# Kernel optimization log

Measured on AMD Instinct MI355X. Metric: run time of the kernel, lower is better.

The kernel has to match this reference:

```python
import jax, jax.numpy as jnp
import numpy as np
from jax import lax

BS, DIM, S, CF, K = 8, 128, 1024, 512, 16384
TAU = 0.2
EPS = 1e-12


def _norm(x, axis):
    # torch F.normalize: x / max(||x||, eps)
    return x / jnp.clip(jnp.linalg.norm(x, axis=axis, keepdims=True), EPS, None)


def setup_inputs() -> dict:
    key = jax.random.key(0)
    ks = jax.random.split(key, 8)
    inp = {
        "g_q": jax.random.normal(ks[0], (BS, DIM), jnp.float32),
        "g_k": jax.random.normal(ks[1], (BS, DIM), jnp.float32),
        "d_q": jax.random.normal(ks[2], (BS, DIM, S), jnp.float32),
        "d_k": jax.random.normal(ks[3], (BS, DIM, S), jnp.float32),
        "feat_q": jax.random.normal(ks[4], (BS, CF, S), jnp.float32),
        "feat_k": jax.random.normal(ks[5], (BS, CF, S), jnp.float32),
        # queues are L2-normalized along dim 0 at module construction
        "queue_g": _norm(jax.random.normal(ks[6], (DIM, K), jnp.float32), 0),
        "queue_d": _norm(jax.random.normal(ks[7], (DIM, K), jnp.float32), 0),
    }
    return inp


def reference(g_q, g_k, d_q, d_k, feat_q, feat_k, queue_g, queue_d):
    g_qn = _norm(g_q, 1)                      # [B, D]
    d_qn = _norm(d_q, 1)                      # [B, D, S]

    # --- torch.no_grad() block: key branch + dense 1-NN match ---
    g_kn = _norm(g_k, 1)                      # [B, D]
    d_kn = _norm(d_k, 1)                      # [B, D, S]
    f_k = _norm(feat_k, 1)                    # [B, C, S]
    f_q = _norm(feat_q, 1)                    # [B, C, S]
    cosine = jnp.einsum('bqi,bqj->bij', f_k, f_q)   # [B, S, S]
    match_idx = jnp.argmax(cosine, axis=1)          # [B, S]
    # gather query dense features at matched indices (detached, as in source)
    d_qg = jnp.take_along_axis(d_qn, match_idx[:, None, :], axis=2)  # [B, D, S]
    g_kn, d_kn, d_qg = lax.stop_gradient((g_kn, d_kn, d_qg))

    # global contrastive logits
    pos_g = jnp.einsum('bd,bd->b', g_qn, g_kn)[:, None]              # [B, 1]
    neg_g = g_qn @ lax.stop_gradient(queue_g)                        # [B, K]
    output_g = jnp.concatenate([pos_g, neg_g], axis=1) / TAU         # [B, 1+K]
    target_g = jnp.zeros((BS,), dtype=jnp.int32)

    # dense contrastive logits
    pos_d = jnp.einsum('bdz,bdz->bz', d_kn, d_qg)[:, None, :]        # [B, 1, S]
    neg_d = jnp.einsum('bdz,dq->bqz', d_qg, lax.stop_gradient(queue_d))  # [B, K, S]
    output_d = jnp.concatenate([pos_d, neg_d], axis=1) / TAU         # [B, 1+K, S]
    target_d = jnp.zeros((BS, S), dtype=jnp.int32)

    return output_g, target_g, output_d, target_d
```

## Files before the change

kernel.cpp:

```cpp
#include <hip/hip_runtime.h>
#include <math.h>
#include <stdint.h>

constexpr int B   = 8;
constexpr int DIM = 128;
constexpr int S   = 1024;
constexpr int CF  = 512;
constexpr int K   = 16384;
constexpr float INV_TAU = 5.0f;
constexpr float EPSF    = 1e-12f;

constexpr int64_t OG_OFF = 0;
constexpr int64_t TG_OFF = (int64_t)B * (K + 1);
constexpr int64_t OD_OFF = TG_OFF + B;
constexpr int64_t TD_OFF = OD_OFF + (int64_t)B * (K + 1) * S;

typedef __attribute__((ext_vector_type(8))) short s16x8;
typedef __attribute__((ext_vector_type(4))) float f32x4;

__device__ inline void split2(float x, uint16_t& h, uint16_t& l) {
    uint32_t bx = __float_as_uint(x);
    h = (uint16_t)(bx >> 16);
    float r = x - __uint_as_float(bx & 0xFFFF0000u);
    l = (uint16_t)(__float_as_uint(r) >> 16);
}

__global__ void zero_targets_kernel(float* out) {
    int t = blockIdx.x * 256 + threadIdx.x;
    if (t < B) out[TG_OFF + t] = 0.0f;
    if (t < B * S) out[TD_OFF + t] = 0.0f;
}

__global__ void g_norm_kernel(const float* __restrict__ g_q,
                              const float* __restrict__ g_k,
                              float* __restrict__ g_qn,
                              float* __restrict__ g_kn,
                              float* __restrict__ out) {
    int b = blockIdx.x;
    int d = threadIdx.x;
    float q = g_q[b * DIM + d];
    float k = g_k[b * DIM + d];
    float sq = q * q, sk = k * k;
#pragma unroll
    for (int off = 32; off > 0; off >>= 1) {
        sq += __shfl_down(sq, off, 64);
        sk += __shfl_down(sk, off, 64);
    }
    __shared__ float red[4];
    int w = d >> 6;
    if ((d & 63) == 0) { red[w] = sq; red[2 + w] = sk; }
    __syncthreads();
    float invq = 1.0f / fmaxf(sqrtf(red[0] + red[1]), EPSF);
    float invk = 1.0f / fmaxf(sqrtf(red[2] + red[3]), EPSF);
    float qn = q * invq, kn = k * invk;
    g_qn[b * DIM + d] = qn;
    g_kn[b * DIM + d] = kn;
    float p = qn * kn;
#pragma unroll
    for (int off = 32; off > 0; off >>= 1) p += __shfl_down(p, off, 64);
    __shared__ float red2[2];
    if ((d & 63) == 0) red2[w] = p;
    __syncthreads();
    if (d == 0) out[OG_OFF + (int64_t)b * (K + 1)] = (red2[0] + red2[1]) * INV_TAU;
}

__global__ void neg_g_kernel(const float* __restrict__ g_qn,
                             const float* __restrict__ queue_g,
                             float* __restrict__ out) {
    __shared__ float gq[B * DIM];
    int t = threadIdx.x;
    for (int i = t; i < B * DIM; i += 256) gq[i] = g_qn[i];
    __syncthreads();
    int k = blockIdx.x * 256 + t;
    float acc[B] = {0, 0, 0, 0, 0, 0, 0, 0};
    for (int d = 0; d < DIM; ++d) {
        float v = queue_g[(int64_t)d * K + k];
#pragma unroll
        for (int b = 0; b < B; ++b) acc[b] = fmaf(gq[b * DIM + d], v, acc[b]);
    }
#pragma unroll
    for (int b = 0; b < B; ++b)
        out[OG_OFF + (int64_t)b * (K + 1) + 1 + k] = acc[b] * INV_TAU;
}

template <int ROWS>
__global__ void invnorm_kernel(const float* __restrict__ x, float* __restrict__ rn) {
    int b = blockIdx.y;
    int s = blockIdx.x * 64 + (threadIdx.x & 63);
    int g = threadIdx.x >> 6;
    const float* base = x + (int64_t)b * ROWS * S + s;
    float acc = 0.0f;
    for (int r = g; r < ROWS; r += 4) {
        float v = base[(int64_t)r * S];
        acc = fmaf(v, v, acc);
    }
    __shared__ float red[256];
    red[threadIdx.x] = acc;
    __syncthreads();
    if (g == 0) {
        int sl = threadIdx.x;
        float tot = red[sl] + red[64 + sl] + red[128 + sl] + red[192 + sl];
        rn[b * S + s] = 1.0f / fmaxf(sqrtf(tot), EPSF);
    }
}

constexpr int CC = 32;
__global__ void cos_argmax_kernel(const float* __restrict__ f_k,
                                  const float* __restrict__ f_q,
                                  const float* __restrict__ rn_fk,
                                  const float* __restrict__ rn_fq,
                                  float* __restrict__ pmax,
                                  int* __restrict__ pidx) {
    int jt = blockIdx.x, ic = blockIdx.y, b = blockIdx.z;
    int j0 = jt * 64;
    int tx = threadIdx.x & 15, ty = threadIdx.x >> 4;
    __shared__ __align__(16) float sk[CC][68];
    __shared__ __align__(16) float sq[CC][68];
    const float* fkb = f_k + (int64_t)b * CF * S;
    const float* fqb = f_q + (int64_t)b * CF * S;

    float bestv[4];
    int besti[4];
#pragma unroll
    for (int jj = 0; jj < 4; ++jj) { bestv[jj] = -INFINITY; besti[jj] = 0; }
    float rq[4];
#pragma unroll
    for (int jj = 0; jj < 4; ++jj) rq[jj] = rn_fq[b * S + j0 + ty * 4 + jj];

    for (int it = 0; it < 4; ++it) {
        int i_base = ic * 256 + it * 64;
        float acc[4][4] = {};
        for (int c0 = 0; c0 < CF; c0 += CC) {
            for (int e = threadIdx.x; e < CC * 64; e += 256) {
                int r = e >> 6, col = e & 63;
                sk[r][col] = fkb[(int64_t)(c0 + r) * S + i_base + col];
                sq[r][col] = fqb[(int64_t)(c0 + r) * S + j0 + col];
            }
            __syncthreads();
#pragma unroll
            for (int r = 0; r < CC; ++r) {
                float4 av4 = *(const float4*)&sk[r][tx * 4];
                float4 bv4 = *(const float4*)&sq[r][ty * 4];
                float a_[4] = {av4.x, av4.y, av4.z, av4.w};
                float b_[4] = {bv4.x, bv4.y, bv4.z, bv4.w};
#pragma unroll
                for (int ii = 0; ii < 4; ++ii)
#pragma unroll
                    for (int jj = 0; jj < 4; ++jj)
                        acc[ii][jj] = fmaf(a_[ii], b_[jj], acc[ii][jj]);
            }
            __syncthreads();
        }
        float rk[4];
#pragma unroll
        for (int ii = 0; ii < 4; ++ii) rk[ii] = rn_fk[b * S + i_base + tx * 4 + ii];
#pragma unroll
        for (int jj = 0; jj < 4; ++jj)
#pragma unroll
            for (int ii = 0; ii < 4; ++ii) {
                float v = acc[ii][jj] * rk[ii] * rq[jj];
                if (v > bestv[jj]) { bestv[jj] = v; besti[jj] = i_base + tx * 4 + ii; }
            }
    }
#pragma unroll
    for (int jj = 0; jj < 4; ++jj) {
        float v = bestv[jj];
        int idx = besti[jj];
#pragma unroll
        for (int off = 8; off > 0; off >>= 1) {
            float ov = __shfl_down(v, off, 16);
            int oi = __shfl_down(idx, off, 16);
            if (ov > v || (ov == v && oi < idx)) { v = ov; idx = oi; }
        }
        if (tx == 0) {
            int j = j0 + ty * 4 + jj;
            pmax[(int64_t)(ic * B + b) * S + j] = v;
            pidx[(int64_t)(ic * B + b) * S + j] = idx;
        }
    }
}

__global__ void argmax_merge_kernel(const float* __restrict__ pmax,
                                    const int* __restrict__ pidx,
                                    int* __restrict__ match) {
    int t = blockIdx.x * 256 + threadIdx.x;
    if (t >= B * S) return;
    int b = t / S, s = t % S;
    float bv = -INFINITY;
    int bi = 0;
    for (int ic = 0; ic < 4; ++ic) {
        float v = pmax[(int64_t)(ic * B + b) * S + s];
        int i = pidx[(int64_t)(ic * B + b) * S + s];
        if (v > bv || (v == bv && i < bi)) { bv = v; bi = i; }
    }
    match[t] = bi;
}

__global__ void queue_split_kernel(const float* __restrict__ qd,
                                   uint16_t* __restrict__ qhi,
                                   uint16_t* __restrict__ qlo) {
    int q0 = blockIdx.x * 64;
    __shared__ float tile[DIM][65];
    for (int e = threadIdx.x; e < DIM * 64; e += 256) {
        int d = e >> 6, c = e & 63;
        tile[d][c] = qd[(int64_t)d * K + q0 + c];
    }
    __syncthreads();
    int qq = threadIdx.x >> 2;
    int dg = threadIdx.x & 3;
    uint16_t* gh = qhi + (int64_t)(q0 + qq) * DIM + dg * 32;
    uint16_t* gl = qlo + (int64_t)(q0 + qq) * DIM + dg * 32;
#pragma unroll
    for (int v = 0; v < 4; ++v) {
        uint32_t ph[4], pl[4];
#pragma unroll
        for (int p = 0; p < 4; ++p) {
            int d = dg * 32 + v * 8 + p * 2;
            uint16_t h0, l0, h1, l1;
            split2(tile[d][qq], h0, l0);
            split2(tile[d + 1][qq], h1, l1);
            ph[p] = (uint32_t)h0 | ((uint32_t)h1 << 16);
            pl[p] = (uint32_t)l0 | ((uint32_t)l1 << 16);
        }
        *(uint4*)(gh + v * 8) = make_uint4(ph[0], ph[1], ph[2], ph[3]);
        *(uint4*)(gl + v * 8) = make_uint4(pl[0], pl[1], pl[2], pl[3]);
    }
}

__global__ void gather_prep_kernel(const float* __restrict__ d_q,
                                   const float* __restrict__ d_k,
                                   const float* __restrict__ rn_dq,
                                   const int* __restrict__ match,
                                   uint16_t* __restrict__ ghi,
                                   uint16_t* __restrict__ glo,
                                   float* __restrict__ out) {
    int b = blockIdx.y, z0 = blockIdx.x * 64;
    int zl = threadIdx.x & 63, dg = threadIdx.x >> 6;
    __shared__ float tile[DIM][65];
    __shared__ float redd[4][64], redn[4][64];
    __shared__ int   sm[64];
    __shared__ float ssc[64];
    if (threadIdx.x < 64) {
        int m = match[b * S + z0 + threadIdx.x];
        sm[threadIdx.x] = m;
        ssc[threadIdx.x] = rn_dq[b * S + m];
    }
    __syncthreads();
    int m = sm[zl];
    float sc = ssc[zl];
    const float* dqb = d_q + (int64_t)b * DIM * S;
    const float* dkb = d_k + (int64_t)b * DIM * S + z0;
    float dot = 0.0f, nk = 0.0f;
    for (int i = 0; i < 32; ++i) {
        int d = dg * 32 + i;
        float val = dqb[(int64_t)d * S + m] * sc;
        float kv  = dkb[(int64_t)d * S + zl];
        tile[d][zl] = val;
        dot = fmaf(kv, val, dot);
        nk  = fmaf(kv, kv, nk);
    }
    redd[dg][zl] = dot;
    redn[dg][zl] = nk;
    __syncthreads();
    if (dg == 0) {
        float D  = redd[0][zl] + redd[1][zl] + redd[2][zl] + redd[3][zl];
        float Nk = redn[0][zl] + redn[1][zl] + redn[2][zl] + redn[3][zl];
        out[OD_OFF + (int64_t)b * (K + 1) * S + z0 + zl] =
            D / fmaxf(sqrtf(Nk), EPSF) * INV_TAU;
    }
    int zz = threadIdx.x >> 2;
    int dg2 = threadIdx.x & 3;
    uint16_t* gh = ghi + ((int64_t)b * S + z0 + zz) * DIM + dg2 * 32;
    uint16_t* gl = glo + ((int64_t)b * S + z0 + zz) * DIM + dg2 * 32;
#pragma unroll
    for (int v = 0; v < 4; ++v) {
        uint32_t ph[4], pl[4];
#pragma unroll
        for (int p = 0; p < 4; ++p) {
            int d = dg2 * 32 + v * 8 + p * 2;
            uint16_t h0, l0, h1, l1;
            split2(tile[d][zz], h0, l0);
            split2(tile[d + 1][zz], h1, l1);
            ph[p] = (uint32_t)h0 | ((uint32_t)h1 << 16);
            pl[p] = (uint32_t)l0 | ((uint32_t)l1 << 16);
        }
        *(uint4*)(gh + v * 8) = make_uint4(ph[0], ph[1], ph[2], ph[3]);
        *(uint4*)(gl + v * 8) = make_uint4(pl[0], pl[1], pl[2], pl[3]);
    }
}

__global__ void neg_d_mfma_kernel(const uint16_t* __restrict__ qhi,
                                  const uint16_t* __restrict__ qlo,
                                  const uint16_t* __restrict__ ghi,
                                  const uint16_t* __restrict__ glo,
                                  float* __restrict__ out) {
    int b = blockIdx.z;
    int q0 = blockIdx.x * 128;
    int z0 = blockIdx.y * 128;
    int wave = threadIdx.x >> 6, lane = threadIdx.x & 63;
    int wq = q0 + (wave >> 1) * 64;
    int wz = z0 + (wave & 1) * 64;
    int r  = lane & 15;
    int kd = (lane >> 4) * 8;

    f32x4 acc[4][4];
    const f32x4 z4 = {0.0f, 0.0f, 0.0f, 0.0f};
#pragma unroll
    for (int i = 0; i < 4; ++i)
#pragma unroll
        for (int j = 0; j < 4; ++j) acc[i][j] = z4;

    const int64_t gbase = (int64_t)b * S;
#pragma unroll
    for (int ds = 0; ds < 4; ++ds) {
        int doff = ds * 32 + kd;
        s16x8 ah[4], al[4], bh[4], bl[4];
#pragma unroll
        for (int i = 0; i < 4; ++i) {
            int64_t arow = (int64_t)(wq + i * 16 + r) * DIM + doff;
            ah[i] = *(const s16x8*)(qhi + arow);
            al[i] = *(const s16x8*)(qlo + arow);
            int64_t brow = (gbase + wz + i * 16 + r) * DIM + doff;
            bh[i] = *(const s16x8*)(ghi + brow);
            bl[i] = *(const s16x8*)(glo + brow);
        }
#pragma unroll
        for (int i = 0; i < 4; ++i)
#pragma unroll
            for (int j = 0; j < 4; ++j)
                acc[i][j] = __builtin_amdgcn_mfma_f32_16x16x32_bf16(ah[i], bh[j], acc[i][j], 0, 0, 0);
#pragma unroll
        for (int i = 0; i < 4; ++i)
#pragma unroll
            for (int j = 0; j < 4; ++j)
                acc[i][j] = __builtin_amdgcn_mfma_f32_16x16x32_bf16(ah[i], bl[j], acc[i][j], 0, 0, 0);
#pragma unroll
        for (int i = 0; i < 4; ++i)
#pragma unroll
            for (int j = 0; j < 4; ++j)
                acc[i][j] = __builtin_amdgcn_mfma_f32_16x16x32_bf16(al[i], bh[j], acc[i][j], 0, 0, 0);
    }

    int col = lane & 15;
    int rb  = (lane >> 4) * 4;
#pragma unroll
    for (int i = 0; i < 4; ++i) {
        int q = wq + i * 16 + rb;
#pragma unroll
        for (int j = 0; j < 4; ++j) {
            int z = wz + j * 16 + col;
            float* o = out + OD_OFF + ((int64_t)b * (K + 1) + 1 + q) * S + z;
#pragma unroll
            for (int reg = 0; reg < 4; ++reg)
                o[(int64_t)reg * S] = acc[i][j][reg] * INV_TAU;
        }
    }
}

extern "C" void kernel_launch(void* const* d_in, const int* in_sizes, int n_in,
                              void* d_out, int out_size, void* d_ws, size_t ws_size,
                              hipStream_t stream) {
    const float* g_q     = (const float*)d_in[0];
    const float* g_k     = (const float*)d_in[1];
    const float* d_q     = (const float*)d_in[2];
    const float* d_k     = (const float*)d_in[3];
    const float* feat_q  = (const float*)d_in[4];
    const float* feat_k  = (const float*)d_in[5];
    const float* queue_g = (const float*)d_in[6];
    const float* queue_d = (const float*)d_in[7];
    float* out = (float*)d_out;

    float* ws    = (float*)d_ws;
    float* g_qn  = ws;
    float* g_kn  = g_qn + 1024;
    float* rn_fq = g_kn + 1024;
    float* rn_fk = rn_fq + B * S;
    float* rn_dq = rn_fk + B * S;
    float* pmax  = rn_dq + B * S;
    int*   pidx  = (int*)(pmax + 4 * B * S);
    int*   match = pidx + 4 * B * S;
    uint16_t* qhi = (uint16_t*)(match + B * S);
    uint16_t* qlo = qhi + (size_t)K * DIM;
    uint16_t* ghi = qlo + (size_t)K * DIM;
    uint16_t* glo = ghi + (size_t)B * S * DIM;

    zero_targets_kernel<<<(B * S + 255) / 256, 256, 0, stream>>>(out);
    g_norm_kernel<<<B, DIM, 0, stream>>>(g_q, g_k, g_qn, g_kn, out);
    neg_g_kernel<<<K / 256, 256, 0, stream>>>(g_qn, queue_g, out);
    queue_split_kernel<<<K / 64, 256, 0, stream>>>(queue_d, qhi, qlo);
    invnorm_kernel<CF><<<dim3(S / 64, B), 256, 0, stream>>>(feat_q, rn_fq);
    invnorm_kernel<CF><<<dim3(S / 64, B), 256, 0, stream>>>(feat_k, rn_fk);
    invnorm_kernel<DIM><<<dim3(S / 64, B), 256, 0, stream>>>(d_q, rn_dq);
    cos_argmax_kernel<<<dim3(S / 64, 4, B), 256, 0, stream>>>(feat_k, feat_q, rn_fk, rn_fq, pmax, pidx);
    argmax_merge_kernel<<<(B * S + 255) / 256, 256, 0, stream>>>(pmax, pidx, match);
    gather_prep_kernel<<<dim3(S / 64, B), 256, 0, stream>>>(d_q, d_k, rn_dq, match, ghi, glo, out);
    neg_d_mfma_kernel<<<dim3(K / 128, S / 128, B), 256, 0, stream>>>(qhi, qlo, ghi, glo, out);
}
```

Baseline: 1.263 ms.

## Stage neg_d MFMA outputs through LDS for float4 stores and remap blocks across XCDs

The neg_d output epilogue now writes accumulator fragments into a per-wave LDS tile and reads them back as contiguous float4 rows. Each global store then covers 64 consecutive floats per row instead of scattered 16-float scalar writes, which targets the write bandwidth of the roughly 540 MB output. The grid is also flattened to 1D, and the block id is remapped so that each group of eight consecutive ids is spread across the (d_id & 7) slices, likely to balance work or locality across XCDs. The change adds LDS usage and block-wide syncs per row group; the syncs are only needed per wave but are taken by the whole block.

```diff
diff --git a/kernel.cpp b/kernel.cpp
--- a/kernel.cpp
+++ b/kernel.cpp
@@ -294,9 +294,15 @@
                                   const uint16_t* __restrict__ ghi,
                                   const uint16_t* __restrict__ glo,
                                   float* __restrict__ out) {
-    int b = blockIdx.z;
-    int q0 = blockIdx.x * 128;
-    int z0 = blockIdx.y * 128;
+    int d_id = blockIdx.x;
+    int work = (d_id & 7) * 1024 + (d_id >> 3);
+    int x = work >> 6;
+    int rem = work & 63;
+    int y = rem & 7;
+    int b = rem >> 3;
+
+    int q0 = x * 128;
+    int z0 = y * 128;
     int wave = threadIdx.x >> 6, lane = threadIdx.x & 63;
     int wq = q0 + (wave >> 1) * 64;
     int wz = z0 + (wave & 1) * 64;
@@ -341,19 +347,28 @@
                 acc[i][j] = __builtin_amdgcn_mfma_f32_16x16x32_bf16(al[i], bh[j], acc[i][j], 0, 0, 0);
     }
 
+    __shared__ __align__(16) float st[4][16][68];
     int col = lane & 15;
     int rb  = (lane >> 4) * 4;
+    int rr  = lane >> 4;
+    int zc  = (lane & 15) * 4;
 #pragma unroll
     for (int i = 0; i < 4; ++i) {
-        int q = wq + i * 16 + rb;
-#pragma unroll
-        for (int j = 0; j < 4; ++j) {
-            int z = wz + j * 16 + col;
-            float* o = out + OD_OFF + ((int64_t)b * (K + 1) + 1 + q) * S + z;
+#pragma unroll
+        for (int j = 0; j < 4; ++j)
 #pragma unroll
             for (int reg = 0; reg < 4; ++reg)
-                o[(int64_t)reg * S] = acc[i][j][reg] * INV_TAU;
-        }
+                st[wave][rb + reg][j * 16 + col] = acc[i][j][reg];
+        __syncthreads();
+#pragma unroll
+        for (int pass = 0; pass < 4; ++pass) {
+            int row = pass * 4 + rr;
+            float4 v = *(const float4*)&st[wave][row][zc];
+            v.x *= INV_TAU; v.y *= INV_TAU; v.z *= INV_TAU; v.w *= INV_TAU;
+            int q = wq + i * 16 + row;
+            *(float4*)&out[OD_OFF + ((int64_t)b * (K + 1) + 1 + q) * S + wz + zc] = v;
+        }
+        __syncthreads();
     }
 }
 
@@ -394,5 +409,5 @@
     cos_argmax_kernel<<<dim3(S / 64, 4, B), 256, 0, stream>>>(feat_k, feat_q, rn_fk, rn_fq, pmax, pidx);
     argmax_merge_kernel<<<(B * S + 255) / 256, 256, 0, stream>>>(pmax, pidx, match);
     gather_prep_kernel<<<dim3(S / 64, B), 256, 0, stream>>>(d_q, d_k, rn_dq, match, ghi, glo, out);
-    neg_d_mfma_kernel<<<dim3(K / 128, S / 128, B), 256, 0, stream>>>(qhi, qlo, ghi, glo, out);
-}
+    neg_d_mfma_kernel<<<8192, 256, 0, stream>>>(qhi, qlo, ghi, glo, out);
+}
```

New measurement: 1.431 ms. 1.13x slower.
